# Performance work log

Measured on AMD Instinct MI355X. Metric: run time of the kernel, lower is better.

The kernel has to match this reference:

```python
import jax, jax.numpy as jnp
import numpy as np

N_NODES = 100000


def _sage_conv(x, edge_index, W_l, W_r, b):
    # PyG SAGEConv (aggr='mean', root_weight=True, bias in lin_l):
    # out_i = W_l @ mean_{j in N(i)} x_j + b + W_r @ x_i
    src = edge_index[0]
    dst = edge_index[1]
    msg = x[src]                                              # [E, d] gather
    agg = jax.ops.segment_sum(msg, dst, num_segments=N_NODES)  # [N, d]
    deg = jax.ops.segment_sum(jnp.ones((src.shape[0],), x.dtype), dst,
                              num_segments=N_NODES)            # [N]
    agg = agg / jnp.maximum(deg, 1.0)[:, None]                 # mean, 0 if isolated
    return agg @ W_l.T + b + x @ W_r.T


def setup_inputs() -> dict:
    key = jax.random.key(0)
    ks = jax.random.split(key, 10)
    E, P = 1600000, 200000
    d_in, d_hid, d_out = 64, 128, 64
    s = 0.05
    return {
        "x": jax.random.normal(ks[0], (N_NODES, d_in), jnp.float32),
        "edge_index": jax.random.randint(ks[1], (2, E), 0, N_NODES, jnp.int32).astype(jnp.int64),
        "pairs": jax.random.randint(ks[2], (P, 2), 0, N_NODES, jnp.int32).astype(jnp.int64),
        "W1l": jax.random.normal(ks[3], (d_hid, d_in), jnp.float32) * s,
        "W1r": jax.random.normal(ks[4], (d_hid, d_in), jnp.float32) * s,
        "b1": jnp.zeros((d_hid,), jnp.float32),
        "W2l": jax.random.normal(ks[5], (d_out, d_hid), jnp.float32) * s,
        "W2r": jax.random.normal(ks[6], (d_out, d_hid), jnp.float32) * s,
        "b2": jnp.zeros((d_out,), jnp.float32),
        "Wlp": jax.random.normal(ks[7], (1, 2 * d_out), jnp.float32) * s,
        "blp": jnp.zeros((1,), jnp.float32),
    }


def reference(x, edge_index, pairs, W1l, W1r, b1, W2l, W2r, b2, Wlp, blp):
    h = _sage_conv(x, edge_index, W1l, W1r, b1)
    h = jax.nn.relu(h)
    h = _sage_conv(h, edge_index, W2l, W2r, b2)          # [N, d_out]
    src_emb = h[pairs[:, 0]]                              # [P, d_out]
    dst_emb = h[pairs[:, 1]]                              # [P, d_out]
    edge_emb = jnp.concatenate([src_emb, dst_emb], axis=1)  # [P, 2*d_out]
    logits = edge_emb @ Wlp.T + blp                       # [P, 1]
    return jax.nn.sigmoid(logits).squeeze(-1)             # [P]
```

## Files before the change

### kernel.cpp

```cpp
#include <hip/hip_runtime.h>


typedef __attribute__((ext_vector_type(8))) short bf16x8;
typedef __attribute__((ext_vector_type(4))) float f32x4;

#define NBLK_A 256

__device__ __forceinline__ unsigned short f2bf(float f) {
    unsigned u = __float_as_uint(f);
    u = u + 0x7fffu + ((u >> 16) & 1u);
    return (unsigned short)(u >> 16);
}
__device__ __forceinline__ float b2f(unsigned short s) {
    return __uint_as_float(((unsigned)s) << 16);
}
__device__ __forceinline__ float uflo(unsigned v) { return __uint_as_float(v << 16); }
__device__ __forceinline__ float ufhi(unsigned v) { return __uint_as_float(v & 0xffff0000u); }

__device__ __forceinline__ long load_idx(const void* p, long i, int is64) {
    if (is64) return (long)((const long long*)p)[i];
    return (long)((const int*)p)[i];
}

__device__ __forceinline__ int detect64_local(const void* p) {
    const unsigned* u = (const unsigned*)p;
    unsigned a = 0;
#pragma unroll
    for (int i = 0; i < 32; ++i) a |= u[2 * i + 1];
    return a == 0u;
}

__global__ void pre_kernel(const void* eidx, const float* __restrict__ x,
                           const float* __restrict__ W1l, const float* __restrict__ W1r,
                           const float* __restrict__ W2l, const float* __restrict__ W2r,
                           const float* __restrict__ b2, const float* __restrict__ Wlp,
                           const float* __restrict__ blp,
                           int* __restrict__ blk_hist, unsigned short* __restrict__ xaown,
                           unsigned short* __restrict__ w1bf, float* __restrict__ wv,
                           int* __restrict__ flag,
                           long N, long E, int NBK, int chunk, int xcb) {
    int b = blockIdx.x;
    int tid = threadIdx.x;
    if (b < NBLK_A) {
        __shared__ int h[512];
        for (int i = tid; i < NBK; i += 256) h[i] = 0;
        __syncthreads();
        int is64 = detect64_local(eidx);
        long e0 = (long)b * chunk;
        long e1 = e0 + chunk; if (e1 > E) e1 = E;
        for (long e = e0 + tid; e < e1; e += 256) {
            long dst = load_idx(eidx, E + e, is64);
            atomicAdd(&h[(int)(dst >> 8)], 1);
        }
        __syncthreads();
        for (int i = tid; i < NBK; i += 256) blk_hist[i * NBLK_A + b] = h[i];
    } else if (b < NBLK_A + xcb) {
        long t = (long)(b - NBLK_A) * 256 + tid;
        long n = t >> 4;
        int q = (int)(t & 15);
        if (n >= N) return;
        float4 v = *(const float4*)&x[n * 64 + q * 4];
        uint2 u;
        u.x = (unsigned)f2bf(v.x) | ((unsigned)f2bf(v.y) << 16);
        u.y = (unsigned)f2bf(v.z) | ((unsigned)f2bf(v.w) << 16);
        *(uint2*)&xaown[n * 64 + q * 4] = u;
    } else {
        if (tid == 0) *flag = detect64_local(eidx);
        if (tid < 128) {
            int k = tid;
            float s0 = 0.f, s1 = 0.f, s2 = 0.f, s3 = 0.f;
            for (int o = 0; o < 64; ++o) {
                float wl = Wlp[o], wr = Wlp[64 + o];
                float l = W2l[o * 128 + k], r = W2r[o * 128 + k];
                s0 += wl * l; s1 += wr * l; s2 += wl * r; s3 += wr * r;
            }
            wv[k] = s0; wv[128 + k] = s1; wv[256 + k] = s2; wv[384 + k] = s3;
            if (k == 0) {
                float c = blp[0];
                for (int o = 0; o < 64; ++o) c += (Wlp[o] + Wlp[64 + o]) * b2[o];
                wv[512] = c;
            }
        }
        for (int i = tid; i < 16384; i += 256) {
            int o = i >> 7, k = i & 127;
            float f = (k < 64) ? W1l[o * 64 + k] : W1r[o * 64 + (k - 64)];
            w1bf[i ^ ((o & 7) << 3)] = f2bf(f);
        }
    }
}

__global__ void bucket_relscan_kernel(int* __restrict__ blk_hist, int* __restrict__ total) {
    __shared__ int ts[256];
    int k = blockIdx.x, t = threadIdx.x;
    int v = blk_hist[k * NBLK_A + t];
    ts[t] = v; __syncthreads();
    for (int off = 1; off < 256; off <<= 1) {
        int u = (t >= off) ? ts[t - off] : 0;
        __syncthreads();
        ts[t] += u;
        __syncthreads();
    }
    blk_hist[k * NBLK_A + t] = ts[t] - v;
    if (t == 255) total[k] = ts[255];
}

__global__ void base_kernel(const int* __restrict__ total, int* __restrict__ base,
                            int* __restrict__ row_start, int NBK, long N, long E) {
    __shared__ int ts[256];
    int t = threadIdx.x;
    int a = (t < NBK) ? total[t] : 0;
    int b = (256 + t < NBK) ? total[256 + t] : 0;
    ts[t] = a; __syncthreads();
    for (int off = 1; off < 256; off <<= 1) {
        int u = (t >= off) ? ts[t - off] : 0;
        __syncthreads();
        ts[t] += u;
        __syncthreads();
    }
    int incl1 = ts[t];
    int sum1 = ts[255];
    if (t < NBK) base[t] = incl1 - a;
    __syncthreads();
    ts[t] = b; __syncthreads();
    for (int off = 1; off < 256; off <<= 1) {
        int u = (t >= off) ? ts[t - off] : 0;
        __syncthreads();
        ts[t] += u;
        __syncthreads();
    }
    int incl2 = ts[t];
    if (256 + t < NBK) base[256 + t] = sum1 + incl2 - b;
    if (t == 255) base[NBK] = sum1 + incl2;
    if (t == 0) row_start[N] = (int)E;
}

__global__ void bucket_scatter_kernel(const void* eidx, const int* flag,
                                      const int* __restrict__ blk_hist, const int* __restrict__ base,
                                      unsigned* __restrict__ ebuf, long E, int NBK, int chunk) {
    __shared__ int cur[512];
    int tid = threadIdx.x, b = blockIdx.x;
    for (int i = tid; i < NBK; i += 256) cur[i] = blk_hist[i * NBLK_A + b] + base[i];
    __syncthreads();
    int is64 = *flag;
    long e0 = (long)b * chunk;
    long e1 = e0 + chunk; if (e1 > E) e1 = E;
    for (long e = e0 + tid; e < e1; e += 256) {
        long src = load_idx(eidx, e, is64);
        long dst = load_idx(eidx, E + e, is64);
        int pos = atomicAdd(&cur[(int)(dst >> 8)], 1);
        ebuf[pos] = (unsigned)src | ((unsigned)(dst & 255) << 24);
    }
}

__global__ void bucket_csr_kernel(const unsigned* __restrict__ ebuf, const int* __restrict__ base,
                                  int* __restrict__ csr_src, int* __restrict__ row_start, long N) {
    __shared__ int cnt[256], sc[256], cur[256];
    int k = blockIdx.x, t = threadIdx.x;
    int bstart = base[k], bend = base[k + 1];
    cnt[t] = 0;
    __syncthreads();
    for (int i = bstart + t; i < bend; i += 256)
        atomicAdd(&cnt[ebuf[i] >> 24], 1);
    __syncthreads();
    int c = cnt[t];
    sc[t] = c; __syncthreads();
    for (int off = 1; off < 256; off <<= 1) {
        int u = (t >= off) ? sc[t - off] : 0;
        __syncthreads();
        sc[t] += u;
        __syncthreads();
    }
    int loff = sc[t] - c;
    cur[t] = loff;
    long n = (long)k * 256 + t;
    if (n < N) row_start[n] = bstart + loff;
    __syncthreads();
    for (int i = bstart + t; i < bend; i += 256) {
        unsigned v = ebuf[i];
        int dl = (int)(v >> 24);
        int p = atomicAdd(&cur[dl], 1);
        csr_src[bstart + p] = (int)(v & 0xFFFFFFu);
    }
}

__global__ void gather_kernel(const int* __restrict__ rs, const int* __restrict__ csr,
                              const unsigned short* __restrict__ T,
                              unsigned short* __restrict__ Out, long N) {
    long gid = (long)blockIdx.x * 256 + threadIdx.x;
    long n = gid >> 6;
    if (n >= N) return;
    int lane = (int)(gid & 63);
    int lg = lane >> 4;
    int fq = lane & 15;
    int s = rs[n], e = rs[n + 1];
    unsigned boff = (unsigned)fq * 4u;
    float a0 = 0.f, a1 = 0.f, a2 = 0.f, a3 = 0.f;
    int j = s;
    for (; j + 16 <= e; j += 16) {
        unsigned o0 = ((unsigned)csr[j + lg] << 6) | boff;
        unsigned o1 = ((unsigned)csr[j + 4 + lg] << 6) | boff;
        unsigned o2 = ((unsigned)csr[j + 8 + lg] << 6) | boff;
        unsigned o3 = ((unsigned)csr[j + 12 + lg] << 6) | boff;
        uint2 r0 = *(const uint2*)&T[o0];
        uint2 r1 = *(const uint2*)&T[o1];
        uint2 r2 = *(const uint2*)&T[o2];
        uint2 r3 = *(const uint2*)&T[o3];
        a0 += uflo(r0.x); a1 += ufhi(r0.x); a2 += uflo(r0.y); a3 += ufhi(r0.y);
        a0 += uflo(r1.x); a1 += ufhi(r1.x); a2 += uflo(r1.y); a3 += ufhi(r1.y);
        a0 += uflo(r2.x); a1 += ufhi(r2.x); a2 += uflo(r2.y); a3 += ufhi(r2.y);
        a0 += uflo(r3.x); a1 += ufhi(r3.x); a2 += uflo(r3.y); a3 += ufhi(r3.y);
    }
    if (j < e) {
#pragma unroll
        for (int t = 0; t < 4; ++t) {
            int pos = j + 4 * t + lg;
            int ok = pos < e;
            unsigned oo = ((unsigned)csr[ok ? pos : s] << 6) | boff;
            uint2 r = *(const uint2*)&T[oo];
            float m = ok ? 1.f : 0.f;
            a0 += m * uflo(r.x); a1 += m * ufhi(r.x);
            a2 += m * uflo(r.y); a3 += m * ufhi(r.y);
        }
    }
    a0 += __shfl_xor(a0, 16, 64);  a1 += __shfl_xor(a1, 16, 64);
    a2 += __shfl_xor(a2, 16, 64);  a3 += __shfl_xor(a3, 16, 64);
    a0 += __shfl_xor(a0, 32, 64);  a1 += __shfl_xor(a1, 32, 64);
    a2 += __shfl_xor(a2, 32, 64);  a3 += __shfl_xor(a3, 32, 64);
    if (lg == 0) {
        float inv = 1.0f / fmaxf((float)(e - s), 1.0f);
        uint2 o;
        o.x = (unsigned)f2bf(a0 * inv) | ((unsigned)f2bf(a1 * inv) << 16);
        o.y = (unsigned)f2bf(a2 * inv) | ((unsigned)f2bf(a3 * inv) << 16);
        *(uint2*)&Out[((unsigned)n << 6) | boff] = o;
    }
}

__global__ __launch_bounds__(512) void fused_gemm_kernel(
        const unsigned short* __restrict__ xagg, const unsigned short* __restrict__ xaown,
        const unsigned short* __restrict__ w1bf, const float* __restrict__ b1,
        const float* __restrict__ wv,
        float* __restrict__ ab, float* __restrict__ cd, long N) {
    __shared__ __align__(16) unsigned short wbuf[128 * 128];
    __shared__ float bs1[128];
    __shared__ float wvs[512];
    int tid = threadIdx.x;

    {
        const uint4* src = (const uint4*)w1bf;
        uint4* dst = (uint4*)wbuf;
#pragma unroll
        for (int i = 0; i < 4; ++i) dst[tid + i * 512] = src[tid + i * 512];
    }
    if (tid < 128) bs1[tid] = b1[tid];
    wvs[tid] = wv[tid];
    __syncthreads();

    int lane = tid & 63, wid = tid >> 6;
    int l16 = lane & 15, lg = lane >> 4;
    long n0 = (long)blockIdx.x * 128 + wid * 16;
    const unsigned short* Ag = xagg + (n0 + l16) * 64;
    const unsigned short* Ao = xaown + (n0 + l16) * 64;

    f32x4 acc[8];
#pragma unroll
    for (int ot = 0; ot < 8; ++ot) acc[ot] = (f32x4){0.f, 0.f, 0.f, 0.f};

#pragma unroll
    for (int ks = 0; ks < 4; ++ks) {
        int k0 = ks * 32;
        bf16x8 a;
        if (ks < 2) a = *(const bf16x8*)&Ag[k0 + 8 * lg];
        else        a = *(const bf16x8*)&Ao[(k0 - 64) + 8 * lg];
#pragma unroll
        for (int ot = 0; ot < 8; ++ot) {
            int o = ot * 16 + l16;
            bf16x8 b = *(const bf16x8*)&wbuf[(o * 128 + k0 + 8 * lg) ^ ((o & 7) << 3)];
            acc[ot] = __builtin_amdgcn_mfma_f32_16x16x32_bf16(a, b, acc[ot], 0, 0, 0);
        }
    }

#pragma unroll
    for (int j = 0; j < 4; ++j) {
        float da = 0.f, db = 0.f, dc = 0.f, dd = 0.f;
#pragma unroll
        for (int ot = 0; ot < 8; ++ot) {
            int col = ot * 16 + l16;
            float hv = fmaxf(acc[ot][j] + bs1[col], 0.f);
            da += hv * wvs[col];       db += hv * wvs[128 + col];
            dc += hv * wvs[256 + col]; dd += hv * wvs[384 + col];
        }
        da += __shfl_xor(da, 1, 64); db += __shfl_xor(db, 1, 64);
        dc += __shfl_xor(dc, 1, 64); dd += __shfl_xor(dd, 1, 64);
        da += __shfl_xor(da, 2, 64); db += __shfl_xor(db, 2, 64);
        dc += __shfl_xor(dc, 2, 64); dd += __shfl_xor(dd, 2, 64);
        da += __shfl_xor(da, 4, 64); db += __shfl_xor(db, 4, 64);
        dc += __shfl_xor(dc, 4, 64); dd += __shfl_xor(dd, 4, 64);
        da += __shfl_xor(da, 8, 64); db += __shfl_xor(db, 8, 64);
        dc += __shfl_xor(dc, 8, 64); dd += __shfl_xor(dd, 8, 64);
        long n = n0 + lg * 4 + j;
        if (l16 == 0 && n < N) {
            *(float2*)&ab[n * 2] = make_float2(da, db);
            *(float2*)&cd[n * 2] = make_float2(dc, dd);
        }
    }
}

__global__ void sgather_kernel(const int* __restrict__ rs, const int* __restrict__ csr,
                               const float* __restrict__ ab, const float* __restrict__ cd,
                               float* __restrict__ UV, long N) {
    long n = (long)blockIdx.x * 256 + threadIdx.x;
    if (n >= N) return;
    int s = rs[n], e = rs[n + 1];
    float sa = 0.f, sb = 0.f;
    int j = s;
    for (; j + 4 <= e; j += 4) {
        unsigned i0 = (unsigned)csr[j] * 2u, i1 = (unsigned)csr[j + 1] * 2u;
        unsigned i2 = (unsigned)csr[j + 2] * 2u, i3 = (unsigned)csr[j + 3] * 2u;
        float2 v0 = *(const float2*)&ab[i0];
        float2 v1 = *(const float2*)&ab[i1];
        float2 v2 = *(const float2*)&ab[i2];
        float2 v3 = *(const float2*)&ab[i3];
        sa += (v0.x + v1.x) + (v2.x + v3.x);
        sb += (v0.y + v1.y) + (v2.y + v3.y);
    }
    for (; j < e; ++j) {
        float2 v = *(const float2*)&ab[(unsigned)csr[j] * 2u];
        sa += v.x; sb += v.y;
    }
    float inv = 1.0f / fmaxf((float)(e - s), 1.0f);
    float2 cdv = *(const float2*)&cd[n * 2];
    *(float2*)&UV[n * 2] = make_float2(sa * inv + cdv.x, sb * inv + cdv.y);
}

__global__ void linkpred_kernel(const void* pairs, const int* flag,
                                const float* __restrict__ UV, const float* __restrict__ wv,
                                float* __restrict__ out, long P) {
    long p = (long)blockIdx.x * 256 + threadIdx.x;
    if (p >= P) return;
    int is64 = *flag;
    long s = load_idx(pairs, 2 * p, is64);
    long d = load_idx(pairs, 2 * p + 1, is64);
    float acc = UV[s * 2] + UV[d * 2 + 1] + wv[512];
    out[p] = 1.0f / (1.0f + expf(-acc));
}

extern "C" void kernel_launch(void* const* d_in, const int* in_sizes, int n_in,
                              void* d_out, int out_size, void* d_ws, size_t ws_size,
                              hipStream_t stream) {
    const float* x    = (const float*)d_in[0];
    const void*  eidx  = d_in[1];
    const void*  pairs = d_in[2];
    const float* W1l = (const float*)d_in[3];
    const float* W1r = (const float*)d_in[4];
    const float* b1  = (const float*)d_in[5];
    const float* W2l = (const float*)d_in[6];
    const float* W2r = (const float*)d_in[7];
    const float* b2  = (const float*)d_in[8];
    const float* Wlp = (const float*)d_in[9];
    const float* blp = (const float*)d_in[10];
    float* out = (float*)d_out;

    long N = in_sizes[0] / 64;
    long E = in_sizes[1] / 2;
    long P = in_sizes[2] / 2;
    long NP = (N + 127) & ~127L;
    int NBK = (int)((N + 255) >> 8);
    int chunk = (int)((E + NBLK_A - 1) / NBLK_A);
    int xcb = (int)((N * 16 + 255) / 256);

    char* w = (char*)d_ws;
    auto alloc = [&](size_t bytes) {
        char* p = w;
        w += (bytes + 255) & ~(size_t)255;
        return p;
    };
    int* row_start = (int*)alloc((N + 1) * sizeof(int));
    int* csr_src   = (int*)alloc(E * sizeof(int));
    int* blk_hist  = (int*)alloc((size_t)NBK * NBLK_A * sizeof(int));
    int* total     = (int*)alloc(NBK * sizeof(int));
    int* base      = (int*)alloc((NBK + 1) * sizeof(int));
    int* flag      = (int*)alloc(64);
    unsigned* ebuf = (unsigned*)alloc(E * sizeof(unsigned));
    unsigned short* xaown = (unsigned short*)alloc((size_t)NP * 64 * 2);
    unsigned short* xagg  = (unsigned short*)alloc((size_t)NP * 64 * 2);
    unsigned short* w1bf  = (unsigned short*)alloc(16384 * 2);
    float* ab = (float*)alloc((size_t)N * 2 * sizeof(float));
    float* cd = (float*)alloc((size_t)N * 2 * sizeof(float));
    float* UV = (float*)alloc((size_t)N * 2 * sizeof(float));
    float* wv = (float*)alloc(1024 * sizeof(float));

    unsigned pre_blocks = (unsigned)(NBLK_A + xcb + 1);
    pre_kernel<<<pre_blocks, 256, 0, stream>>>(eidx, x, W1l, W1r, W2l, W2r, b2, Wlp, blp,
                                               blk_hist, xaown, w1bf, wv, flag,
                                               N, E, NBK, chunk, xcb);

    bucket_relscan_kernel<<<NBK, 256, 0, stream>>>(blk_hist, total);
    base_kernel<<<1, 256, 0, stream>>>(total, base, row_start, NBK, N, E);
    bucket_scatter_kernel<<<NBLK_A, 256, 0, stream>>>(eidx, flag, blk_hist, base, ebuf, E, NBK, chunk);
    bucket_csr_kernel<<<NBK, 256, 0, stream>>>(ebuf, base, csr_src, row_start, N);

    unsigned gth_blocks = (unsigned)((N * 64 + 255) / 256);
    gather_kernel<<<gth_blocks, 256, 0, stream>>>(row_start, csr_src, xaown, xagg, N);

    unsigned gblocks = (unsigned)(NP / 128);
    fused_gemm_kernel<<<gblocks, 512, 0, stream>>>(xagg, xaown, w1bf, b1, wv, ab, cd, N);

    unsigned sgblocks = (unsigned)((N + 255) / 256);
    sgather_kernel<<<sgblocks, 256, 0, stream>>>(row_start, csr_src, ab, cd, UV, N);

    unsigned pblocks = (unsigned)((P + 255) / 256);
    linkpred_kernel<<<pblocks, 256, 0, stream>>>(pairs, flag, UV, wv, out, P);
}
```

Baseline: 131.7 us.

## Fuse bucket scan and base with last-block pattern, cache CSR buckets in LDS

Merges the per-bucket relative scan and the global base scan into one kernel. A done counter, reset in pre_kernel, lets the last finishing block compute the bases, which removes one kernel launch. The histogram and scatter loops now handle two edges per thread, with the chunk size rounded to an even number. The CSR kernel stages each bucket's entries in LDS so ebuf is read from global memory once, falling back to the old path for oversized buckets. The trade-off is extra threadfence and atomic overhead, plus a 20KB LDS array that may lower occupancy.

```diff
diff --git a/kernel.cpp b/kernel.cpp
--- a/kernel.cpp
+++ b/kernel.cpp
@@ -5,6 +5,7 @@
 typedef __attribute__((ext_vector_type(4))) float f32x4;
 
 #define NBLK_A 256
+#define CSR_LDS_CAP 5120
 
 __device__ __forceinline__ unsigned short f2bf(float f) {
     unsigned u = __float_as_uint(f);
@@ -37,7 +38,7 @@
                            const float* __restrict__ blp,
                            int* __restrict__ blk_hist, unsigned short* __restrict__ xaown,
                            unsigned short* __restrict__ w1bf, float* __restrict__ wv,
-                           int* __restrict__ flag,
+                           int* __restrict__ flag, int* __restrict__ done,
                            long N, long E, int NBK, int chunk, int xcb) {
     int b = blockIdx.x;
     int tid = threadIdx.x;
@@ -48,9 +49,16 @@
         int is64 = detect64_local(eidx);
         long e0 = (long)b * chunk;
         long e1 = e0 + chunk; if (e1 > E) e1 = E;
-        for (long e = e0 + tid; e < e1; e += 256) {
-            long dst = load_idx(eidx, E + e, is64);
-            atomicAdd(&h[(int)(dst >> 8)], 1);
+        long e = e0 + tid * 2;
+        for (; e + 1 < e1; e += 512) {
+            long d0 = load_idx(eidx, E + e, is64);
+            long d1 = load_idx(eidx, E + e + 1, is64);
+            atomicAdd(&h[(int)(d0 >> 8)], 1);
+            atomicAdd(&h[(int)(d1 >> 8)], 1);
+        }
+        if (e < e1) {
+            long d0 = load_idx(eidx, E + e, is64);
+            atomicAdd(&h[(int)(d0 >> 8)], 1);
         }
         __syncthreads();
         for (int i = tid; i < NBK; i += 256) blk_hist[i * NBLK_A + b] = h[i];
@@ -65,7 +73,7 @@
         u.y = (unsigned)f2bf(v.z) | ((unsigned)f2bf(v.w) << 16);
         *(uint2*)&xaown[n * 64 + q * 4] = u;
     } else {
-        if (tid == 0) *flag = detect64_local(eidx);
+        if (tid == 0) { *flag = detect64_local(eidx); *done = 0; }
         if (tid < 128) {
             int k = tid;
             float s0 = 0.f, s1 = 0.f, s2 = 0.f, s3 = 0.f;
@@ -89,8 +97,11 @@
     }
 }
 
-__global__ void bucket_relscan_kernel(int* __restrict__ blk_hist, int* __restrict__ total) {
+__global__ void relscan_base_kernel(int* __restrict__ blk_hist, int* __restrict__ total,
+                                    int* __restrict__ base, int* __restrict__ row_start,
+                                    int* __restrict__ done, int NBK, long N, long E) {
     __shared__ int ts[256];
+    __shared__ int isLast;
     int k = blockIdx.x, t = threadIdx.x;
     int v = blk_hist[k * NBLK_A + t];
     ts[t] = v; __syncthreads();
@@ -102,12 +113,12 @@
     }
     blk_hist[k * NBLK_A + t] = ts[t] - v;
     if (t == 255) total[k] = ts[255];
-}
-
-__global__ void base_kernel(const int* __restrict__ total, int* __restrict__ base,
-                            int* __restrict__ row_start, int NBK, long N, long E) {
-    __shared__ int ts[256];
-    int t = threadIdx.x;
+    __threadfence();
+    __syncthreads();
+    if (t == 0) isLast = (atomicAdd(done, 1) == gridDim.x - 1);
+    __syncthreads();
+    if (!isLast) return;
+    __threadfence();
     int a = (t < NBK) ? total[t] : 0;
     int b = (256 + t < NBK) ? total[256 + t] : 0;
     ts[t] = a; __syncthreads();
@@ -144,23 +155,44 @@
     int is64 = *flag;
     long e0 = (long)b * chunk;
     long e1 = e0 + chunk; if (e1 > E) e1 = E;
-    for (long e = e0 + tid; e < e1; e += 256) {
-        long src = load_idx(eidx, e, is64);
-        long dst = load_idx(eidx, E + e, is64);
-        int pos = atomicAdd(&cur[(int)(dst >> 8)], 1);
-        ebuf[pos] = (unsigned)src | ((unsigned)(dst & 255) << 24);
+    long e = e0 + tid * 2;
+    for (; e + 1 < e1; e += 512) {
+        long s0 = load_idx(eidx, e, is64);
+        long s1 = load_idx(eidx, e + 1, is64);
+        long d0 = load_idx(eidx, E + e, is64);
+        long d1 = load_idx(eidx, E + e + 1, is64);
+        int p0 = atomicAdd(&cur[(int)(d0 >> 8)], 1);
+        ebuf[p0] = (unsigned)s0 | ((unsigned)(d0 & 255) << 24);
+        int p1 = atomicAdd(&cur[(int)(d1 >> 8)], 1);
+        ebuf[p1] = (unsigned)s1 | ((unsigned)(d1 & 255) << 24);
+    }
+    if (e < e1) {
+        long s0 = load_idx(eidx, e, is64);
+        long d0 = load_idx(eidx, E + e, is64);
+        int p0 = atomicAdd(&cur[(int)(d0 >> 8)], 1);
+        ebuf[p0] = (unsigned)s0 | ((unsigned)(d0 & 255) << 24);
     }
 }
 
 __global__ void bucket_csr_kernel(const unsigned* __restrict__ ebuf, const int* __restrict__ base,
                                   int* __restrict__ csr_src, int* __restrict__ row_start, long N) {
+    __shared__ unsigned eL[CSR_LDS_CAP];
     __shared__ int cnt[256], sc[256], cur[256];
     int k = blockIdx.x, t = threadIdx.x;
     int bstart = base[k], bend = base[k + 1];
+    int m = bend - bstart;
     cnt[t] = 0;
     __syncthreads();
-    for (int i = bstart + t; i < bend; i += 256)
-        atomicAdd(&cnt[ebuf[i] >> 24], 1);
+    if (m <= CSR_LDS_CAP) {
+        for (int i = t; i < m; i += 256) {
+            unsigned v = ebuf[bstart + i];
+            eL[i] = v;
+            atomicAdd(&cnt[v >> 24], 1);
+        }
+    } else {
+        for (int i = bstart + t; i < bend; i += 256)
+            atomicAdd(&cnt[ebuf[i] >> 24], 1);
+    }
     __syncthreads();
     int c = cnt[t];
     sc[t] = c; __syncthreads();
@@ -175,11 +207,18 @@
     long n = (long)k * 256 + t;
     if (n < N) row_start[n] = bstart + loff;
     __syncthreads();
-    for (int i = bstart + t; i < bend; i += 256) {
-        unsigned v = ebuf[i];
-        int dl = (int)(v >> 24);
-        int p = atomicAdd(&cur[dl], 1);
-        csr_src[bstart + p] = (int)(v & 0xFFFFFFu);
+    if (m <= CSR_LDS_CAP) {
+        for (int i = t; i < m; i += 256) {
+            unsigned v = eL[i];
+            int p = atomicAdd(&cur[v >> 24], 1);
+            csr_src[bstart + p] = (int)(v & 0xFFFFFFu);
+        }
+    } else {
+        for (int i = bstart + t; i < bend; i += 256) {
+            unsigned v = ebuf[i];
+            int p = atomicAdd(&cur[v >> 24], 1);
+            csr_src[bstart + p] = (int)(v & 0xFFFFFFu);
+        }
     }
 }
 
@@ -365,7 +404,7 @@
     long P = in_sizes[2] / 2;
     long NP = (N + 127) & ~127L;
     int NBK = (int)((N + 255) >> 8);
-    int chunk = (int)((E + NBLK_A - 1) / NBLK_A);
+    int chunk = (int)(((E + NBLK_A - 1) / NBLK_A + 1) & ~1L);
     int xcb = (int)((N * 16 + 255) / 256);
 
     char* w = (char*)d_ws;
@@ -380,6 +419,7 @@
     int* total     = (int*)alloc(NBK * sizeof(int));
     int* base      = (int*)alloc((NBK + 1) * sizeof(int));
     int* flag      = (int*)alloc(64);
+    int* done      = (int*)alloc(64);
     unsigned* ebuf = (unsigned*)alloc(E * sizeof(unsigned));
     unsigned short* xaown = (unsigned short*)alloc((size_t)NP * 64 * 2);
     unsigned short* xagg  = (unsigned short*)alloc((size_t)NP * 64 * 2);
@@ -391,11 +431,10 @@
 
     unsigned pre_blocks = (unsigned)(NBLK_A + xcb + 1);
     pre_kernel<<<pre_blocks, 256, 0, stream>>>(eidx, x, W1l, W1r, W2l, W2r, b2, Wlp, blp,
-                                               blk_hist, xaown, w1bf, wv, flag,
+                                               blk_hist, xaown, w1bf, wv, flag, done,
                                                N, E, NBK, chunk, xcb);
 
-    bucket_relscan_kernel<<<NBK, 256, 0, stream>>>(blk_hist, total);
-    base_kernel<<<1, 256, 0, stream>>>(total, base, row_start, NBK, N, E);
+    relscan_base_kernel<<<NBK, 256, 0, stream>>>(blk_hist, total, base, row_start, done, NBK, N, E);
     bucket_scatter_kernel<<<NBLK_A, 256, 0, stream>>>(eidx, flag, blk_hist, base, ebuf, E, NBK, chunk);
     bucket_csr_kernel<<<NBK, 256, 0, stream>>>(ebuf, base, csr_src, row_start, N);
 
```

Measured after the change: 154.7 us. 1.17x slower.
